# Kernel tuning notes

Measured on AMD Instinct MI355X. Metric: run time of the kernel, lower is better.

## Reference

```python
import jax, jax.numpy as jnp
import numpy as np

H = 256
V = 50257
L = 2048
B = 32


def setup_inputs() -> dict:
    key = jax.random.key(0)
    ks = jax.random.split(key, 14)
    s = 0.05  # weight scale
    return {
        "tokens": jax.random.randint(ks[0], (B,), 0, V),
        "hidden": jax.random.normal(ks[1], (1, B, H), jnp.float32),
        "cell": jax.random.normal(ks[2], (1, B, H), jnp.float32),
        "encoder_outputs": jax.random.normal(ks[3], (B, L, H), jnp.float32),
        "emb_table": jax.random.normal(ks[4], (V, H), jnp.float32) * s,
        "W_attn": jax.random.normal(ks[5], (H, 2 * H), jnp.float32) * s,
        "b_attn": jax.random.normal(ks[6], (H,), jnp.float32) * s,
        "v": jax.random.normal(ks[7], (H,), jnp.float32) * s,
        "W_ih": jax.random.normal(ks[8], (4 * H, 2 * H), jnp.float32) * s,
        "b_ih": jax.random.normal(ks[9], (4 * H,), jnp.float32) * s,
        "W_hh": jax.random.normal(ks[10], (4 * H, H), jnp.float32) * s,
        "b_hh": jax.random.normal(ks[11], (4 * H,), jnp.float32) * s,
        "W_out": jax.random.normal(ks[12], (V, 2 * H), jnp.float32) * s,
        "b_out": jax.random.normal(ks[13], (V,), jnp.float32) * s,
    }


def reference(tokens, hidden, cell, encoder_outputs, emb_table, W_attn, b_attn, v,
              W_ih, b_ih, W_hh, b_hh, W_out, b_out):
    # embedded: (B, H); dropout is identity in eval mode
    embedded = emb_table[tokens]
    h_last = hidden[-1]  # (B, H)

    # Bahdanau-style energy: attn(cat(h, e)) then dot with v (NO tanh, per source)
    # split the 2H-input linear into hidden part and encoder part
    Wh, We = W_attn[:, :H], W_attn[:, H:]
    eh = h_last @ Wh.T                                      # (B, H)
    ee = jnp.einsum('blh,kh->blk', encoder_outputs, We)     # (B, L, H)
    energy = eh[:, None, :] + ee + b_attn                   # (B, L, H)
    scores = energy @ v                                     # (B, L)
    attn_weights = jax.nn.softmax(scores, axis=-1)          # (B, L)

    # context = bmm(attn_weights, encoder_outputs)
    attn_applied = jnp.einsum('bl,blh->bh', attn_weights, encoder_outputs)  # (B, H)

    # single-step LSTM, input = cat(embedded, context): (B, 2H)
    x = jnp.concatenate([embedded, attn_applied], axis=-1)
    gates = x @ W_ih.T + b_ih + hidden[0] @ W_hh.T + b_hh   # (B, 4H)
    i_g, f_g, g_g, o_g = jnp.split(gates, 4, axis=-1)
    c_new = jax.nn.sigmoid(f_g) * cell[0] + jax.nn.sigmoid(i_g) * jnp.tanh(g_g)
    h_new = jax.nn.sigmoid(o_g) * jnp.tanh(c_new)           # (B, H)

    # output projection on cat(lstm_out, context): (B, 2H) -> (B, V)
    logits = jnp.concatenate([h_new, attn_applied], axis=-1) @ W_out.T + b_out
    log_probs = jax.nn.log_softmax(logits, axis=-1)

    return (log_probs, h_new[None], c_new[None], attn_weights[:, None, :])
```

## Files before the change

### kernel.cpp

```cpp
#include <hip/hip_runtime.h>
#include <cstddef>

#define H   256
#define L   2048
#define B   32
#define V   50257
#define H2  512
#define H4  1024
#define CH  64
#define NCH (L/CH)

#define LP_OFF 0
#define HN_OFF (B*V)
#define CN_OFF (HN_OFF + B*H)
#define AW_OFF (CN_OFF + B*H)

#define WS_WP    0
#define WS_XG    (WS_WP + 32*256)
#define WS_XL    (WS_XG + B*H2)
#define WS_S     (WS_XL + B*H2)
#define WS_AV    (WS_S + B*L)
#define WS_AM    (WS_AV + B*NCH*H)
#define WS_AZ    (WS_AM + B*NCH)
#define WS_GATES (WS_AZ + B*NCH)
#define WS_PM    (WS_GATES + B*H4)
#define WS_PZ    (WS_PM + 12800)
#define WS_M     (WS_PZ + 12800)
#define WS_LZ    (WS_M + 32)

#define NBLK_LOG 393

typedef __attribute__((ext_vector_type(8))) short bf16x8;
typedef __attribute__((ext_vector_type(4))) float f32x4;

__device__ inline unsigned short f2bf(float f) {
    unsigned u = __builtin_bit_cast(unsigned, f);
    u += 0x7FFFu + ((u >> 16) & 1u);
    return (unsigned short)(u >> 16);
}

__global__ __launch_bounds__(256) void k_prep(const float* __restrict__ W_attn,
                                              const float* __restrict__ v,
                                              float* __restrict__ ws) {
    int p = blockIdx.x, t = threadIdx.x;
    const float* base = W_attn + H + t;
    float acc = 0.f;
    #pragma unroll
    for (int kk = 0; kk < 8; kk++) {
        int k = p * 8 + kk;
        acc += v[k] * base[(size_t)k * H2];
    }
    ws[WS_WP + p * 256 + t] = acc;
}

__global__ __launch_bounds__(256) void k_attn_flash(const float* __restrict__ enc,
                                                    float* __restrict__ ws) {
    int bid = blockIdx.x;
    int b = bid >> 5, chunk = bid & (NCH - 1);
    int t = threadIdx.x;
    int wave = t >> 6, lane = t & 63;
    int g = lane >> 4, u = lane & 15;
    __shared__ float w_s[256];
    __shared__ float s_lds[CH];
    __shared__ float p_lds[CH];
    __shared__ float red[CH];
    __shared__ float vec_lds[4][256];

    float wsum = 0.f;
    #pragma unroll 8
    for (int p = 0; p < 32; p++) wsum += ws[WS_WP + p * 256 + t];
    w_s[t] = wsum;
    __syncthreads();

    size_t rowbase = (size_t)b * L + chunk * CH;
    const float4* w4s = (const float4*)w_s;
    float4 w0 = w4s[u], w1 = w4s[16 + u], w2 = w4s[32 + u], w3 = w4s[48 + u];

    #pragma unroll
    for (int ir = 0; ir < 4; ir++) {
        int rl = wave * 16 + ir * 4 + g;
        const float4* e4 = (const float4*)(enc + (rowbase + rl) * H);
        float4 a0 = e4[u], a1 = e4[16 + u], a2 = e4[32 + u], a3 = e4[48 + u];
        float p = a0.x * w0.x + a0.y * w0.y + a0.z * w0.z + a0.w * w0.w
                + a1.x * w1.x + a1.y * w1.y + a1.z * w1.z + a1.w * w1.w
                + a2.x * w2.x + a2.y * w2.y + a2.z * w2.z + a2.w * w2.w
                + a3.x * w3.x + a3.y * w3.y + a3.z * w3.z + a3.w * w3.w;
        p += __shfl_down(p, 8); p += __shfl_down(p, 4);
        p += __shfl_down(p, 2); p += __shfl_down(p, 1);
        if (u == 0) s_lds[rl] = p;
    }
    __syncthreads();

    if (t < CH) red[t] = s_lds[t];
    __syncthreads();
    for (int off = 32; off; off >>= 1) { if (t < off) red[t] = fmaxf(red[t], red[t + off]); __syncthreads(); }
    float m = red[0];
    __syncthreads();
    if (t < CH) {
        float e = __expf(s_lds[t] - m);
        p_lds[t] = e; red[t] = e;
        ws[WS_S + rowbase + t] = s_lds[t];
    }
    __syncthreads();
    for (int off = 32; off; off >>= 1) { if (t < off) red[t] += red[t + off]; __syncthreads(); }

    float4 acc = make_float4(0.f, 0.f, 0.f, 0.f);
    const float4* ebase = (const float4*)(enc + (rowbase + wave * 16) * H);
    #pragma unroll 4
    for (int i = 0; i < 16; i++) {
        float p = p_lds[wave * 16 + i];
        float4 a = ebase[i * 64 + lane];
        acc.x += p * a.x; acc.y += p * a.y; acc.z += p * a.z; acc.w += p * a.w;
    }
    *(float4*)&vec_lds[wave][lane * 4] = acc;
    __syncthreads();
    ws[WS_AV + (size_t)bid * 256 + t] = vec_lds[0][t] + vec_lds[1][t] + vec_lds[2][t] + vec_lds[3][t];
    if (t == 0) { ws[WS_AM + bid] = m; ws[WS_AZ + bid] = red[0]; }
}

__global__ __launch_bounds__(256) void k_attn_comb(const int* __restrict__ tokens,
                                                   const float* __restrict__ emb,
                                                   float* __restrict__ ws,
                                                   float* __restrict__ out) {
    int b = blockIdx.x, t = threadIdx.x;
    __shared__ float mc[NCH], zc[NCH];
    if (t < NCH) { mc[t] = ws[WS_AM + b * NCH + t]; zc[t] = ws[WS_AZ + b * NCH + t]; }
    __syncthreads();
    float M = -1e30f;
    #pragma unroll
    for (int c = 0; c < NCH; c++) M = fmaxf(M, mc[c]);
    float Z = 0.f;
    #pragma unroll
    for (int c = 0; c < NCH; c++) Z += zc[c] * __expf(mc[c] - M);
    float inv = 1.f / Z;
    float acc = 0.f;
    #pragma unroll 8
    for (int c = 0; c < NCH; c++) acc += __expf(mc[c] - M) * ws[WS_AV + (size_t)(b * NCH + c) * 256 + t];
    acc *= inv;
    ws[WS_XG + b * H2 + H + t] = acc;
    ws[WS_XL + b * H2 + H + t] = acc;
    int tok = tokens[b];
    ws[WS_XG + b * H2 + t] = emb[(size_t)tok * H + t];
    #pragma unroll
    for (int j = 0; j < 8; j++) {
        int l = t + 256 * j;
        out[AW_OFF + (size_t)b * L + l] = __expf(ws[WS_S + (size_t)b * L + l] - M) * inv;
    }
}

__global__ __launch_bounds__(256) void k_gates(const float* __restrict__ W_ih, const float* __restrict__ b_ih,
                                               const float* __restrict__ W_hh, const float* __restrict__ b_hh,
                                               const float* __restrict__ hidden, float* __restrict__ ws) {
    int t = threadIdx.x;
    int wave = t >> 6, lane = t & 63;
    int o = blockIdx.x * 4 + wave;
    int b = o >> 10, j = o & 1023;
    const float4* wi = (const float4*)(W_ih + (size_t)j * H2);
    const float4* xg = (const float4*)(ws + WS_XG + (size_t)b * H2);
    float4 a0 = wi[lane * 2], a1 = wi[lane * 2 + 1];
    float4 x0 = xg[lane * 2], x1 = xg[lane * 2 + 1];
    float p = a0.x * x0.x + a0.y * x0.y + a0.z * x0.z + a0.w * x0.w
            + a1.x * x1.x + a1.y * x1.y + a1.z * x1.z + a1.w * x1.w;
    const float4* wh = (const float4*)(W_hh + (size_t)j * H);
    const float4* hp = (const float4*)(hidden + (size_t)b * H);
    float4 a2 = wh[lane], x2 = hp[lane];
    p += a2.x * x2.x + a2.y * x2.y + a2.z * x2.z + a2.w * x2.w;
    #pragma unroll
    for (int off = 32; off; off >>= 1) p += __shfl_down(p, off);
    if (lane == 0) ws[WS_GATES + o] = p + b_ih[j] + b_hh[j];
}

__global__ __launch_bounds__(256) void k_lstm(const float* __restrict__ cell,
                                              float* __restrict__ ws, float* __restrict__ out) {
    int b = blockIdx.x, t = threadIdx.x;
    const float* g = ws + WS_GATES + (size_t)b * H4;
    float ig = g[t], fg = g[H + t], gg = g[2 * H + t], og = g[3 * H + t];
    float c = cell[(size_t)b * H + t];
    float si = 1.f / (1.f + expf(-ig));
    float sf = 1.f / (1.f + expf(-fg));
    float so = 1.f / (1.f + expf(-og));
    float cn = sf * c + si * tanhf(gg);
    float hn = so * tanhf(cn);
    out[HN_OFF + b * H + t] = hn;
    out[CN_OFF + b * H + t] = cn;
    ws[WS_XL + b * H2 + t] = hn;
}

__global__ __launch_bounds__(256) void k_logits(const float* __restrict__ W_out,
                                                const float* __restrict__ b_out,
                                                float* __restrict__ ws,
                                                float* __restrict__ out) {
    __shared__ unsigned short Xl[32 * 520];
    int t = threadIdx.x;
    const float4* xl4 = (const float4*)(ws + WS_XL);
    #pragma unroll
    for (int it = 0; it < 16; it++) {
        int fi = t + 256 * it;
        int b = fi >> 7, kq = fi & 127;
        float4 xv = xl4[b * 128 + kq];
        unsigned p0 = (unsigned)f2bf(xv.x) | ((unsigned)f2bf(xv.y) << 16);
        unsigned p1 = (unsigned)f2bf(xv.z) | ((unsigned)f2bf(xv.w) << 16);
        unsigned* dst = (unsigned*)&Xl[b * 520 + kq * 4];
        dst[0] = p0; dst[1] = p1;
    }
    __syncthreads();

    int wave = t >> 6, lane = t & 63, quad = lane >> 4, m = lane & 15;
    int rbase = blockIdx.x * 128 + wave * 32;
    f32x4 zero4 = {0.f, 0.f, 0.f, 0.f};
    f32x4 acc[2][2];
    acc[0][0] = zero4; acc[0][1] = zero4; acc[1][0] = zero4; acc[1][1] = zero4;

    int r0 = rbase + m;
    int r1 = rbase + 16 + m;
    bool v0 = r0 < V, v1 = r1 < V;
    const float* wp0 = W_out + (size_t)r0 * H2 + quad * 8;
    const float* wp1 = W_out + (size_t)r1 * H2 + quad * 8;

    for (int kp = 0; kp < 16; kp++) {
        int k0 = kp * 32;
        bf16x8 a0 = {0,0,0,0,0,0,0,0}, a1 = {0,0,0,0,0,0,0,0};
        if (v0) {
            float4 lo = *(const float4*)(wp0 + k0);
            float4 hi = *(const float4*)(wp0 + k0 + 4);
            a0[0]=(short)f2bf(lo.x); a0[1]=(short)f2bf(lo.y); a0[2]=(short)f2bf(lo.z); a0[3]=(short)f2bf(lo.w);
            a0[4]=(short)f2bf(hi.x); a0[5]=(short)f2bf(hi.y); a0[6]=(short)f2bf(hi.z); a0[7]=(short)f2bf(hi.w);
        }
        if (v1) {
            float4 lo = *(const float4*)(wp1 + k0);
            float4 hi = *(const float4*)(wp1 + k0 + 4);
            a1[0]=(short)f2bf(lo.x); a1[1]=(short)f2bf(lo.y); a1[2]=(short)f2bf(lo.z); a1[3]=(short)f2bf(lo.w);
            a1[4]=(short)f2bf(hi.x); a1[5]=(short)f2bf(hi.y); a1[6]=(short)f2bf(hi.z); a1[7]=(short)f2bf(hi.w);
        }
        bf16x8 b0 = *(bf16x8*)&Xl[(size_t)m * 520 + k0 + quad * 8];
        bf16x8 b1 = *(bf16x8*)&Xl[(size_t)(16 + m) * 520 + k0 + quad * 8];
        acc[0][0] = __builtin_amdgcn_mfma_f32_16x16x32_bf16(a0, b0, acc[0][0], 0, 0, 0);
        acc[0][1] = __builtin_amdgcn_mfma_f32_16x16x32_bf16(a0, b1, acc[0][1], 0, 0, 0);
        acc[1][0] = __builtin_amdgcn_mfma_f32_16x16x32_bf16(a1, b0, acc[1][0], 0, 0, 0);
        acc[1][1] = __builtin_amdgcn_mfma_f32_16x16x32_bf16(a1, b1, acc[1][1], 0, 0, 0);
    }

    float val[2][2][4];
    #pragma unroll
    for (int s = 0; s < 2; s++) {
        #pragma unroll
        for (int i = 0; i < 4; i++) {
            int rr = rbase + s * 16 + quad * 4 + i;
            float bo = (rr < V) ? b_out[rr] : 0.f;
            #pragma unroll
            for (int nt = 0; nt < 2; nt++) {
                float vv = acc[s][nt][i] + bo;
                if (rr < V) {
                    int bcol = nt * 16 + m;
                    out[(size_t)bcol * V + rr] = vv;
                    val[s][nt][i] = vv;
                } else {
                    val[s][nt][i] = -1e30f;
                }
            }
        }
    }
    float pm[2], pz[2];
    #pragma unroll
    for (int nt = 0; nt < 2; nt++) {
        float mx = -1e30f;
        #pragma unroll
        for (int s = 0; s < 2; s++)
            #pragma unroll
            for (int i = 0; i < 4; i++) mx = fmaxf(mx, val[s][nt][i]);
        float sm = 0.f;
        #pragma unroll
        for (int s = 0; s < 2; s++)
            #pragma unroll
            for (int i = 0; i < 4; i++) sm += __expf(val[s][nt][i] - mx);
        pm[nt] = mx; pz[nt] = sm;
    }
    #pragma unroll
    for (int off = 16; off <= 32; off <<= 1) {
        #pragma unroll
        for (int nt = 0; nt < 2; nt++) {
            float om = __shfl_xor(pm[nt], off);
            float oz = __shfl_xor(pz[nt], off);
            float nm = fmaxf(pm[nt], om);
            pz[nt] = pz[nt] * __expf(pm[nt] - nm) + oz * __expf(om - nm);
            pm[nt] = nm;
        }
    }
    __syncthreads();
    float* red = (float*)Xl;
    if (quad == 0) {
        #pragma unroll
        for (int nt = 0; nt < 2; nt++) {
            red[wave * 32 + nt * 16 + m]       = pm[nt];
            red[128 + wave * 32 + nt * 16 + m] = pz[nt];
        }
    }
    __syncthreads();
    if (t < 32) {
        float mf = -1e30f;
        #pragma unroll
        for (int w = 0; w < 4; w++) mf = fmaxf(mf, red[w * 32 + t]);
        float z = 0.f;
        #pragma unroll
        for (int w = 0; w < 4; w++) z += red[128 + w * 32 + t] * __expf(red[w * 32 + t] - mf);
        ws[WS_PM + t * 400 + blockIdx.x] = mf;
        ws[WS_PZ + t * 400 + blockIdx.x] = z;
    }
}

__global__ __launch_bounds__(256) void k_lsm_comb(float* __restrict__ ws) {
    int b = blockIdx.x, t = threadIdx.x;
    float m = -1e30f, z = 0.f;
    for (int i = t; i < NBLK_LOG; i += 256) {
        float mi = ws[WS_PM + b * 400 + i];
        float zi = ws[WS_PZ + b * 400 + i];
        float nm = fmaxf(m, mi);
        z = z * __expf(m - nm) + zi * __expf(mi - nm);
        m = nm;
    }
    __shared__ float rm[256], rz[256];
    rm[t] = m; rz[t] = z; __syncthreads();
    for (int off = 128; off; off >>= 1) {
        if (t < off) {
            float m2 = rm[t + off], z2 = rz[t + off];
            float nm = fmaxf(rm[t], m2);
            rz[t] = rz[t] * __expf(rm[t] - nm) + z2 * __expf(m2 - nm);
            rm[t] = nm;
        }
        __syncthreads();
    }
    if (t == 0) { ws[WS_M + b] = rm[0]; ws[WS_LZ + b] = logf(rz[0]); }
}

__global__ __launch_bounds__(256) void k_lsm_final(const float* __restrict__ ws, float* __restrict__ out) {
    int b = blockIdx.y;
    int r = blockIdx.x * 256 + threadIdx.x;
    if (r < V) {
        size_t i = (size_t)b * V + r;
        out[i] = out[i] - ws[WS_M + b] - ws[WS_LZ + b];
    }
}

extern "C" void kernel_launch(void* const* d_in, const int* in_sizes, int n_in,
                              void* d_out, int out_size, void* d_ws, size_t ws_size,
                              hipStream_t stream) {
    const int*   tokens = (const int*)d_in[0];
    const float* hidden = (const float*)d_in[1];
    const float* cell   = (const float*)d_in[2];
    const float* enc    = (const float*)d_in[3];
    const float* emb    = (const float*)d_in[4];
    const float* W_attn = (const float*)d_in[5];
    const float* v      = (const float*)d_in[7];
    const float* W_ih   = (const float*)d_in[8];
    const float* b_ih   = (const float*)d_in[9];
    const float* W_hh   = (const float*)d_in[10];
    const float* b_hh   = (const float*)d_in[11];
    const float* W_out  = (const float*)d_in[12];
    const float* b_out  = (const float*)d_in[13];
    float* out = (float*)d_out;
    float* ws  = (float*)d_ws;

    k_prep<<<32, 256, 0, stream>>>(W_attn, v, ws);
    k_attn_flash<<<B * NCH, 256, 0, stream>>>(enc, ws);
    k_attn_comb<<<B, 256, 0, stream>>>(tokens, emb, ws, out);
    k_gates<<<(B * H4) / 4, 256, 0, stream>>>(W_ih, b_ih, W_hh, b_hh, hidden, ws);
    k_lstm<<<B, 256, 0, stream>>>(cell, ws, out);
    k_logits<<<NBLK_LOG, 256, 0, stream>>>(W_out, b_out, ws, out);
    k_lsm_comb<<<B, 256, 0, stream>>>(ws);
    k_lsm_final<<<dim3((V + 255) / 256, B), 256, 0, stream>>>(ws, out);
}
```

Before: 289.8 us.

## Fuse attention prep, LSTM gates and log-softmax stages to cut kernel launches

Folds the W_attn·v precompute into each attention block, which now recomputes it redundantly. The attention combine, gate GEMV and LSTM cell are merged into one kernel of 512 blocks, each handling 16 hidden units per batch row. The log-softmax combine is merged into the final normalization, so each block re-reduces the 393 partials and then handles 1024 columns. In k_logits the out-of-range rows are clamped instead of branched on, which drops divergent loads. Together these go from eight launches to four, at the cost of redundant recomputation (256x256 W_attn reads per attention block, partial reductions repeated per block).

```diff
diff --git a/kernel.cpp b/kernel.cpp
--- a/kernel.cpp
+++ b/kernel.cpp
@@ -15,18 +15,13 @@
 #define CN_OFF (HN_OFF + B*H)
 #define AW_OFF (CN_OFF + B*H)
 
-#define WS_WP    0
-#define WS_XG    (WS_WP + 32*256)
-#define WS_XL    (WS_XG + B*H2)
+#define WS_XL    0
 #define WS_S     (WS_XL + B*H2)
 #define WS_AV    (WS_S + B*L)
 #define WS_AM    (WS_AV + B*NCH*H)
 #define WS_AZ    (WS_AM + B*NCH)
-#define WS_GATES (WS_AZ + B*NCH)
-#define WS_PM    (WS_GATES + B*H4)
+#define WS_PM    (WS_AZ + B*NCH)
 #define WS_PZ    (WS_PM + 12800)
-#define WS_M     (WS_PZ + 12800)
-#define WS_LZ    (WS_M + 32)
 
 #define NBLK_LOG 393
 
@@ -39,37 +34,34 @@
     return (unsigned short)(u >> 16);
 }
 
-__global__ __launch_bounds__(256) void k_prep(const float* __restrict__ W_attn,
+__global__ __launch_bounds__(256) void k_attn(const float* __restrict__ W_attn,
                                               const float* __restrict__ v,
+                                              const float* __restrict__ enc,
                                               float* __restrict__ ws) {
-    int p = blockIdx.x, t = threadIdx.x;
-    const float* base = W_attn + H + t;
-    float acc = 0.f;
-    #pragma unroll
-    for (int kk = 0; kk < 8; kk++) {
-        int k = p * 8 + kk;
-        acc += v[k] * base[(size_t)k * H2];
-    }
-    ws[WS_WP + p * 256 + t] = acc;
-}
-
-__global__ __launch_bounds__(256) void k_attn_flash(const float* __restrict__ enc,
-                                                    float* __restrict__ ws) {
     int bid = blockIdx.x;
     int b = bid >> 5, chunk = bid & (NCH - 1);
     int t = threadIdx.x;
     int wave = t >> 6, lane = t & 63;
     int g = lane >> 4, u = lane & 15;
-    __shared__ float w_s[256];
+    __shared__ float v_s[H];
+    __shared__ float w_s[H];
     __shared__ float s_lds[CH];
     __shared__ float p_lds[CH];
     __shared__ float red[CH];
     __shared__ float vec_lds[4][256];
 
-    float wsum = 0.f;
-    #pragma unroll 8
-    for (int p = 0; p < 32; p++) wsum += ws[WS_WP + p * 256 + t];
-    w_s[t] = wsum;
+    v_s[t] = v[t];
+    __syncthreads();
+    {
+        const float* base = W_attn + H + t;
+        float wa = 0.f, wb = 0.f;
+        #pragma unroll 8
+        for (int k = 0; k < H; k += 2) {
+            wa += v_s[k]     * base[(size_t)k * H2];
+            wb += v_s[k + 1] * base[(size_t)(k + 1) * H2];
+        }
+        w_s[t] = wa + wb;
+    }
     __syncthreads();
 
     size_t rowbase = (size_t)b * L + chunk * CH;
@@ -118,14 +110,31 @@
     if (t == 0) { ws[WS_AM + bid] = m; ws[WS_AZ + bid] = red[0]; }
 }
 
-__global__ __launch_bounds__(256) void k_attn_comb(const int* __restrict__ tokens,
-                                                   const float* __restrict__ emb,
-                                                   float* __restrict__ ws,
-                                                   float* __restrict__ out) {
-    int b = blockIdx.x, t = threadIdx.x;
+__global__ __launch_bounds__(256) void k_fuse(const int* __restrict__ tokens,
+                                              const float* __restrict__ emb,
+                                              const float* __restrict__ hidden,
+                                              const float* __restrict__ cell,
+                                              const float* __restrict__ W_ih,
+                                              const float* __restrict__ b_ih,
+                                              const float* __restrict__ W_hh,
+                                              const float* __restrict__ b_hh,
+                                              float* __restrict__ ws,
+                                              float* __restrict__ out) {
+    int blk = blockIdx.x;
+    int b = blk >> 4, s = blk & 15;
+    int t = threadIdx.x;
+    int wave = t >> 6, lane = t & 63;
     __shared__ float mc[NCH], zc[NCH];
+    __shared__ float xs[H2];
+    __shared__ float hs[H];
+    __shared__ float gl[64];
+
     if (t < NCH) { mc[t] = ws[WS_AM + b * NCH + t]; zc[t] = ws[WS_AZ + b * NCH + t]; }
-    __syncthreads();
+    hs[t] = hidden[(size_t)b * H + t];
+    int tok = tokens[b];
+    xs[t] = emb[(size_t)tok * H + t];
+    __syncthreads();
+
     float M = -1e30f;
     #pragma unroll
     for (int c = 0; c < NCH; c++) M = fmaxf(M, mc[c]);
@@ -135,55 +144,52 @@
     float inv = 1.f / Z;
     float acc = 0.f;
     #pragma unroll 8
-    for (int c = 0; c < NCH; c++) acc += __expf(mc[c] - M) * ws[WS_AV + (size_t)(b * NCH + c) * 256 + t];
+    for (int c = 0; c < NCH; c++) acc += __expf(mc[c] - M) * ws[WS_AV + (size_t)(b * NCH + c) * H + t];
     acc *= inv;
-    ws[WS_XG + b * H2 + H + t] = acc;
-    ws[WS_XL + b * H2 + H + t] = acc;
-    int tok = tokens[b];
-    ws[WS_XG + b * H2 + t] = emb[(size_t)tok * H + t];
-    #pragma unroll
-    for (int j = 0; j < 8; j++) {
-        int l = t + 256 * j;
-        out[AW_OFF + (size_t)b * L + l] = __expf(ws[WS_S + (size_t)b * L + l] - M) * inv;
-    }
-}
-
-__global__ __launch_bounds__(256) void k_gates(const float* __restrict__ W_ih, const float* __restrict__ b_ih,
-                                               const float* __restrict__ W_hh, const float* __restrict__ b_hh,
-                                               const float* __restrict__ hidden, float* __restrict__ ws) {
-    int t = threadIdx.x;
-    int wave = t >> 6, lane = t & 63;
-    int o = blockIdx.x * 4 + wave;
-    int b = o >> 10, j = o & 1023;
-    const float4* wi = (const float4*)(W_ih + (size_t)j * H2);
-    const float4* xg = (const float4*)(ws + WS_XG + (size_t)b * H2);
-    float4 a0 = wi[lane * 2], a1 = wi[lane * 2 + 1];
-    float4 x0 = xg[lane * 2], x1 = xg[lane * 2 + 1];
-    float p = a0.x * x0.x + a0.y * x0.y + a0.z * x0.z + a0.w * x0.w
-            + a1.x * x1.x + a1.y * x1.y + a1.z * x1.z + a1.w * x1.w;
-    const float4* wh = (const float4*)(W_hh + (size_t)j * H);
-    const float4* hp = (const float4*)(hidden + (size_t)b * H);
-    float4 a2 = wh[lane], x2 = hp[lane];
-    p += a2.x * x2.x + a2.y * x2.y + a2.z * x2.z + a2.w * x2.w;
-    #pragma unroll
-    for (int off = 32; off; off >>= 1) p += __shfl_down(p, off);
-    if (lane == 0) ws[WS_GATES + o] = p + b_ih[j] + b_hh[j];
-}
-
-__global__ __launch_bounds__(256) void k_lstm(const float* __restrict__ cell,
-                                              float* __restrict__ ws, float* __restrict__ out) {
-    int b = blockIdx.x, t = threadIdx.x;
-    const float* g = ws + WS_GATES + (size_t)b * H4;
-    float ig = g[t], fg = g[H + t], gg = g[2 * H + t], og = g[3 * H + t];
-    float c = cell[(size_t)b * H + t];
-    float si = 1.f / (1.f + expf(-ig));
-    float sf = 1.f / (1.f + expf(-fg));
-    float so = 1.f / (1.f + expf(-og));
-    float cn = sf * c + si * tanhf(gg);
-    float hn = so * tanhf(cn);
-    out[HN_OFF + b * H + t] = hn;
-    out[CN_OFF + b * H + t] = cn;
-    ws[WS_XL + b * H2 + t] = hn;
+    xs[H + t] = acc;
+    if (s == 0) {
+        ws[WS_XL + b * H2 + H + t] = acc;
+        #pragma unroll
+        for (int j = 0; j < 8; j++) {
+            int l = t + 256 * j;
+            out[AW_OFF + (size_t)b * L + l] = __expf(ws[WS_S + (size_t)b * L + l] - M) * inv;
+        }
+    }
+    __syncthreads();
+
+    int ts = s * 16;
+    const float4* xs4 = (const float4*)xs;
+    const float4* hs4 = (const float4*)hs;
+    float4 x0 = xs4[lane * 2], x1 = xs4[lane * 2 + 1];
+    float4 xh = hs4[lane];
+    for (int it = 0; it < 16; it++) {
+        int j = (wave << 8) + ts + it;
+        const float4* wi = (const float4*)(W_ih + (size_t)j * H2);
+        float4 a0 = wi[lane * 2], a1 = wi[lane * 2 + 1];
+        const float4* wh = (const float4*)(W_hh + (size_t)j * H);
+        float4 a2 = wh[lane];
+        float p = a0.x * x0.x + a0.y * x0.y + a0.z * x0.z + a0.w * x0.w
+                + a1.x * x1.x + a1.y * x1.y + a1.z * x1.z + a1.w * x1.w
+                + a2.x * xh.x + a2.y * xh.y + a2.z * xh.z + a2.w * xh.w;
+        #pragma unroll
+        for (int off = 32; off; off >>= 1) p += __shfl_down(p, off);
+        if (lane == 0) gl[wave * 16 + it] = p + b_ih[j] + b_hh[j];
+    }
+    __syncthreads();
+
+    if (t < 16) {
+        int tt = ts + t;
+        float ig = gl[t], fg = gl[16 + t], gg = gl[32 + t], og = gl[48 + t];
+        float c = cell[(size_t)b * H + tt];
+        float si = 1.f / (1.f + expf(-ig));
+        float sf = 1.f / (1.f + expf(-fg));
+        float so = 1.f / (1.f + expf(-og));
+        float cn = sf * c + si * tanhf(gg);
+        float hn = so * tanhf(cn);
+        out[HN_OFF + b * H + tt] = hn;
+        out[CN_OFF + b * H + tt] = cn;
+        ws[WS_XL + b * H2 + tt] = hn;
+    }
 }
 
 __global__ __launch_bounds__(256) void k_logits(const float* __restrict__ W_out,
@@ -213,25 +219,22 @@
 
     int r0 = rbase + m;
     int r1 = rbase + 16 + m;
-    bool v0 = r0 < V, v1 = r1 < V;
-    const float* wp0 = W_out + (size_t)r0 * H2 + quad * 8;
-    const float* wp1 = W_out + (size_t)r1 * H2 + quad * 8;
+    int r0c = r0 < V ? r0 : V - 1;
+    int r1c = r1 < V ? r1 : V - 1;
+    const float* wp0 = W_out + (size_t)r0c * H2 + quad * 8;
+    const float* wp1 = W_out + (size_t)r1c * H2 + quad * 8;
 
     for (int kp = 0; kp < 16; kp++) {
         int k0 = kp * 32;
-        bf16x8 a0 = {0,0,0,0,0,0,0,0}, a1 = {0,0,0,0,0,0,0,0};
-        if (v0) {
-            float4 lo = *(const float4*)(wp0 + k0);
-            float4 hi = *(const float4*)(wp0 + k0 + 4);
-            a0[0]=(short)f2bf(lo.x); a0[1]=(short)f2bf(lo.y); a0[2]=(short)f2bf(lo.z); a0[3]=(short)f2bf(lo.w);
-            a0[4]=(short)f2bf(hi.x); a0[5]=(short)f2bf(hi.y); a0[6]=(short)f2bf(hi.z); a0[7]=(short)f2bf(hi.w);
-        }
-        if (v1) {
-            float4 lo = *(const float4*)(wp1 + k0);
-            float4 hi = *(const float4*)(wp1 + k0 + 4);
-            a1[0]=(short)f2bf(lo.x); a1[1]=(short)f2bf(lo.y); a1[2]=(short)f2bf(lo.z); a1[3]=(short)f2bf(lo.w);
-            a1[4]=(short)f2bf(hi.x); a1[5]=(short)f2bf(hi.y); a1[6]=(short)f2bf(hi.z); a1[7]=(short)f2bf(hi.w);
-        }
+        float4 lo0 = *(const float4*)(wp0 + k0);
+        float4 hi0 = *(const float4*)(wp0 + k0 + 4);
+        float4 lo1 = *(const float4*)(wp1 + k0);
+        float4 hi1 = *(const float4*)(wp1 + k0 + 4);
+        bf16x8 a0, a1;
+        a0[0]=(short)f2bf(lo0.x); a0[1]=(short)f2bf(lo0.y); a0[2]=(short)f2bf(lo0.z); a0[3]=(short)f2bf(lo0.w);
+        a0[4]=(short)f2bf(hi0.x); a0[5]=(short)f2bf(hi0.y); a0[6]=(short)f2bf(hi0.z); a0[7]=(short)f2bf(hi0.w);
+        a1[0]=(short)f2bf(lo1.x); a1[1]=(short)f2bf(lo1.y); a1[2]=(short)f2bf(lo1.z); a1[3]=(short)f2bf(lo1.w);
+        a1[4]=(short)f2bf(hi1.x); a1[5]=(short)f2bf(hi1.y); a1[6]=(short)f2bf(hi1.z); a1[7]=(short)f2bf(hi1.w);
         bf16x8 b0 = *(bf16x8*)&Xl[(size_t)m * 520 + k0 + quad * 8];
         bf16x8 b1 = *(bf16x8*)&Xl[(size_t)(16 + m) * 520 + k0 + quad * 8];
         acc[0][0] = __builtin_amdgcn_mfma_f32_16x16x32_bf16(a0, b0, acc[0][0], 0, 0, 0);
@@ -308,8 +311,10 @@
     }
 }
 
-__global__ __launch_bounds__(256) void k_lsm_comb(float* __restrict__ ws) {
-    int b = blockIdx.x, t = threadIdx.x;
+__global__ __launch_bounds__(256) void k_lsm_final(const float* __restrict__ ws,
+                                                   float* __restrict__ out) {
+    int b = blockIdx.y, t = threadIdx.x;
+    __shared__ float rm[256], rz[256];
     float m = -1e30f, z = 0.f;
     for (int i = t; i < NBLK_LOG; i += 256) {
         float mi = ws[WS_PM + b * 400 + i];
@@ -318,7 +323,6 @@
         z = z * __expf(m - nm) + zi * __expf(mi - nm);
         m = nm;
     }
-    __shared__ float rm[256], rz[256];
     rm[t] = m; rz[t] = z; __syncthreads();
     for (int off = 128; off; off >>= 1) {
         if (t < off) {
@@ -329,15 +333,15 @@
         }
         __syncthreads();
     }
-    if (t == 0) { ws[WS_M + b] = rm[0]; ws[WS_LZ + b] = logf(rz[0]); }
-}
-
-__global__ __launch_bounds__(256) void k_lsm_final(const float* __restrict__ ws, float* __restrict__ out) {
-    int b = blockIdx.y;
-    int r = blockIdx.x * 256 + threadIdx.x;
-    if (r < V) {
-        size_t i = (size_t)b * V + r;
-        out[i] = out[i] - ws[WS_M + b] - ws[WS_LZ + b];
+    float M = rm[0], LZ = logf(rz[0]);
+    int rbase = blockIdx.x * 1024 + t;
+    #pragma unroll
+    for (int j = 0; j < 4; j++) {
+        int r = rbase + 256 * j;
+        if (r < V) {
+            size_t i = (size_t)b * V + r;
+            out[i] = out[i] - M - LZ;
+        }
     }
 }
 
@@ -360,12 +364,8 @@
     float* out = (float*)d_out;
     float* ws  = (float*)d_ws;
 
-    k_prep<<<32, 256, 0, stream>>>(W_attn, v, ws);
-    k_attn_flash<<<B * NCH, 256, 0, stream>>>(enc, ws);
-    k_attn_comb<<<B, 256, 0, stream>>>(tokens, emb, ws, out);
-    k_gates<<<(B * H4) / 4, 256, 0, stream>>>(W_ih, b_ih, W_hh, b_hh, hidden, ws);
-    k_lstm<<<B, 256, 0, stream>>>(cell, ws, out);
+    k_attn<<<B * NCH, 256, 0, stream>>>(W_attn, v, enc, ws);
+    k_fuse<<<B * 16, 256, 0, stream>>>(tokens, emb, hidden, cell, W_ih, b_ih, W_hh, b_hh, ws, out);
     k_logits<<<NBLK_LOG, 256, 0, stream>>>(W_out, b_out, ws, out);
-    k_lsm_comb<<<B, 256, 0, stream>>>(ws);
-    k_lsm_final<<<dim3((V + 255) / 256, B), 256, 0, stream>>>(ws, out);
-}
+    k_lsm_final<<<dim3((V + 1023) / 1024, B), 256, 0, stream>>>(ws, out);
+}
```

After: 297.2 us. 2.6% more time.

## Halve logits rows per block and software-prefetch W_out three steps ahead

Applied to the files above, without the earlier changes.

The logits GEMV kernel now gives each wave 16 vocabulary rows instead of 32, doubling the grid to 786 blocks, and the partial-softmax workspace grows to match. The K loop is fully unrolled with a 3-deep register prefetch of W_out rows, and out-of-range rows are clamped rather than branched, so more global loads are in flight while the MFMAs run. This targets latency hiding in the memory-bound W_out stream. In exchange it adds more blocks, re-stages X into LDS for every block, and doubles the per-block partial results that the combine kernel has to reduce.

```diff
diff --git a/kernel.cpp b/kernel.cpp
--- a/kernel.cpp
+++ b/kernel.cpp
@@ -24,11 +24,11 @@
 #define WS_AZ    (WS_AM + B*NCH)
 #define WS_GATES (WS_AZ + B*NCH)
 #define WS_PM    (WS_GATES + B*H4)
-#define WS_PZ    (WS_PM + 12800)
-#define WS_M     (WS_PZ + 12800)
+#define WS_PZ    (WS_PM + 32*800)
+#define WS_M     (WS_PZ + 32*800)
 #define WS_LZ    (WS_M + 32)
 
-#define NBLK_LOG 393
+#define NBLK_LOG 786
 
 typedef __attribute__((ext_vector_type(8))) short bf16x8;
 typedef __attribute__((ext_vector_type(4))) float f32x4;
@@ -191,88 +191,68 @@
                                                 float* __restrict__ ws,
                                                 float* __restrict__ out) {
     __shared__ unsigned short Xl[32 * 520];
+    __shared__ float red2[256];
     int t = threadIdx.x;
     const float4* xl4 = (const float4*)(ws + WS_XL);
     #pragma unroll
     for (int it = 0; it < 16; it++) {
         int fi = t + 256 * it;
-        int b = fi >> 7, kq = fi & 127;
-        float4 xv = xl4[b * 128 + kq];
+        int bb = fi >> 7, kq = fi & 127;
+        float4 xv = xl4[bb * 128 + kq];
         unsigned p0 = (unsigned)f2bf(xv.x) | ((unsigned)f2bf(xv.y) << 16);
         unsigned p1 = (unsigned)f2bf(xv.z) | ((unsigned)f2bf(xv.w) << 16);
-        unsigned* dst = (unsigned*)&Xl[b * 520 + kq * 4];
+        unsigned* dst = (unsigned*)&Xl[bb * 520 + kq * 4];
         dst[0] = p0; dst[1] = p1;
     }
     __syncthreads();
 
     int wave = t >> 6, lane = t & 63, quad = lane >> 4, m = lane & 15;
-    int rbase = blockIdx.x * 128 + wave * 32;
-    f32x4 zero4 = {0.f, 0.f, 0.f, 0.f};
-    f32x4 acc[2][2];
-    acc[0][0] = zero4; acc[0][1] = zero4; acc[1][0] = zero4; acc[1][1] = zero4;
-
+    int rbase = blockIdx.x * 64 + wave * 16;
     int r0 = rbase + m;
-    int r1 = rbase + 16 + m;
-    bool v0 = r0 < V, v1 = r1 < V;
-    const float* wp0 = W_out + (size_t)r0 * H2 + quad * 8;
-    const float* wp1 = W_out + (size_t)r1 * H2 + quad * 8;
-
+    int rc = r0 < V ? r0 : V - 1;
+    const float4* wq = (const float4*)(W_out + (size_t)rc * H2 + quad * 8);
+
+    f32x4 acc0 = {0.f, 0.f, 0.f, 0.f}, acc1 = {0.f, 0.f, 0.f, 0.f};
+
+    float4 pl0 = wq[0],  ph0 = wq[1];
+    float4 pl1 = wq[8],  ph1 = wq[9];
+    float4 pl2 = wq[16], ph2 = wq[17];
+    #pragma unroll
     for (int kp = 0; kp < 16; kp++) {
         int k0 = kp * 32;
-        bf16x8 a0 = {0,0,0,0,0,0,0,0}, a1 = {0,0,0,0,0,0,0,0};
-        if (v0) {
-            float4 lo = *(const float4*)(wp0 + k0);
-            float4 hi = *(const float4*)(wp0 + k0 + 4);
-            a0[0]=(short)f2bf(lo.x); a0[1]=(short)f2bf(lo.y); a0[2]=(short)f2bf(lo.z); a0[3]=(short)f2bf(lo.w);
-            a0[4]=(short)f2bf(hi.x); a0[5]=(short)f2bf(hi.y); a0[6]=(short)f2bf(hi.z); a0[7]=(short)f2bf(hi.w);
-        }
-        if (v1) {
-            float4 lo = *(const float4*)(wp1 + k0);
-            float4 hi = *(const float4*)(wp1 + k0 + 4);
-            a1[0]=(short)f2bf(lo.x); a1[1]=(short)f2bf(lo.y); a1[2]=(short)f2bf(lo.z); a1[3]=(short)f2bf(lo.w);
-            a1[4]=(short)f2bf(hi.x); a1[5]=(short)f2bf(hi.y); a1[6]=(short)f2bf(hi.z); a1[7]=(short)f2bf(hi.w);
-        }
+        bf16x8 a;
+        a[0]=(short)f2bf(pl0.x); a[1]=(short)f2bf(pl0.y); a[2]=(short)f2bf(pl0.z); a[3]=(short)f2bf(pl0.w);
+        a[4]=(short)f2bf(ph0.x); a[5]=(short)f2bf(ph0.y); a[6]=(short)f2bf(ph0.z); a[7]=(short)f2bf(ph0.w);
         bf16x8 b0 = *(bf16x8*)&Xl[(size_t)m * 520 + k0 + quad * 8];
         bf16x8 b1 = *(bf16x8*)&Xl[(size_t)(16 + m) * 520 + k0 + quad * 8];
-        acc[0][0] = __builtin_amdgcn_mfma_f32_16x16x32_bf16(a0, b0, acc[0][0], 0, 0, 0);
-        acc[0][1] = __builtin_amdgcn_mfma_f32_16x16x32_bf16(a0, b1, acc[0][1], 0, 0, 0);
-        acc[1][0] = __builtin_amdgcn_mfma_f32_16x16x32_bf16(a1, b0, acc[1][0], 0, 0, 0);
-        acc[1][1] = __builtin_amdgcn_mfma_f32_16x16x32_bf16(a1, b1, acc[1][1], 0, 0, 0);
-    }
-
-    float val[2][2][4];
-    #pragma unroll
-    for (int s = 0; s < 2; s++) {
-        #pragma unroll
-        for (int i = 0; i < 4; i++) {
-            int rr = rbase + s * 16 + quad * 4 + i;
-            float bo = (rr < V) ? b_out[rr] : 0.f;
-            #pragma unroll
-            for (int nt = 0; nt < 2; nt++) {
-                float vv = acc[s][nt][i] + bo;
-                if (rr < V) {
-                    int bcol = nt * 16 + m;
-                    out[(size_t)bcol * V + rr] = vv;
-                    val[s][nt][i] = vv;
-                } else {
-                    val[s][nt][i] = -1e30f;
-                }
-            }
-        }
+        acc0 = __builtin_amdgcn_mfma_f32_16x16x32_bf16(a, b0, acc0, 0, 0, 0);
+        acc1 = __builtin_amdgcn_mfma_f32_16x16x32_bf16(a, b1, acc1, 0, 0, 0);
+        pl0 = pl1; ph0 = ph1;
+        pl1 = pl2; ph1 = ph2;
+        if (kp < 13) { pl2 = wq[(kp + 3) * 8]; ph2 = wq[(kp + 3) * 8 + 1]; }
+    }
+
+    float val[2][4];
+    #pragma unroll
+    for (int i = 0; i < 4; i++) {
+        int rr = rbase + quad * 4 + i;
+        float bo = (rr < V) ? b_out[rr] : 0.f;
+        float v0 = acc0[i] + bo, v1 = acc1[i] + bo;
+        if (rr < V) {
+            out[(size_t)m * V + rr]        = v0;
+            out[(size_t)(16 + m) * V + rr] = v1;
+            val[0][i] = v0; val[1][i] = v1;
+        } else { val[0][i] = -1e30f; val[1][i] = -1e30f; }
     }
     float pm[2], pz[2];
     #pragma unroll
     for (int nt = 0; nt < 2; nt++) {
         float mx = -1e30f;
         #pragma unroll
-        for (int s = 0; s < 2; s++)
-            #pragma unroll
-            for (int i = 0; i < 4; i++) mx = fmaxf(mx, val[s][nt][i]);
+        for (int i = 0; i < 4; i++) mx = fmaxf(mx, val[nt][i]);
         float sm = 0.f;
         #pragma unroll
-        for (int s = 0; s < 2; s++)
-            #pragma unroll
-            for (int i = 0; i < 4; i++) sm += __expf(val[s][nt][i] - mx);
+        for (int i = 0; i < 4; i++) sm += __expf(val[nt][i] - mx);
         pm[nt] = mx; pz[nt] = sm;
     }
     #pragma unroll
@@ -287,24 +267,23 @@
         }
     }
     __syncthreads();
-    float* red = (float*)Xl;
     if (quad == 0) {
         #pragma unroll
         for (int nt = 0; nt < 2; nt++) {
-            red[wave * 32 + nt * 16 + m]       = pm[nt];
-            red[128 + wave * 32 + nt * 16 + m] = pz[nt];
+            red2[wave * 32 + nt * 16 + m]       = pm[nt];
+            red2[128 + wave * 32 + nt * 16 + m] = pz[nt];
         }
     }
     __syncthreads();
     if (t < 32) {
         float mf = -1e30f;
         #pragma unroll
-        for (int w = 0; w < 4; w++) mf = fmaxf(mf, red[w * 32 + t]);
+        for (int w = 0; w < 4; w++) mf = fmaxf(mf, red2[w * 32 + t]);
         float z = 0.f;
         #pragma unroll
-        for (int w = 0; w < 4; w++) z += red[128 + w * 32 + t] * __expf(red[w * 32 + t] - mf);
-        ws[WS_PM + t * 400 + blockIdx.x] = mf;
-        ws[WS_PZ + t * 400 + blockIdx.x] = z;
+        for (int w = 0; w < 4; w++) z += red2[128 + w * 32 + t] * __expf(red2[w * 32 + t] - mf);
+        ws[WS_PM + t * 800 + blockIdx.x] = mf;
+        ws[WS_PZ + t * 800 + blockIdx.x] = z;
     }
 }
 
@@ -312,8 +291,8 @@
     int b = blockIdx.x, t = threadIdx.x;
     float m = -1e30f, z = 0.f;
     for (int i = t; i < NBLK_LOG; i += 256) {
-        float mi = ws[WS_PM + b * 400 + i];
-        float zi = ws[WS_PZ + b * 400 + i];
+        float mi = ws[WS_PM + b * 800 + i];
+        float zi = ws[WS_PZ + b * 800 + i];
         float nm = fmaxf(m, mi);
         z = z * __expf(m - nm) + zi * __expf(mi - nm);
         m = nm;
```

After: 294.7 us. No clear change (+1.7%).

## Pre-convert W_out to bf16 in the attention kernel and read bf16 in logits

Applied to the files above, without the earlier changes.

The attention kernel now also converts all of W_out from fp32 to bf16 into a new workspace region, split evenly across its 1024 blocks. The logits kernel then reads half as many bytes of bf16 weights and skips per-element conversion, and clamps out-of-range rows instead of branching. The intent is to move the conversion off the logits critical path and let it run alongside the latency-bound attention pass. The cost is that every call still reads the full fp32 matrix and adds a 51 MB write plus a second read. An fp32-reading fallback kernel runs when the workspace is too small.

```diff
diff --git a/kernel.cpp b/kernel.cpp
--- a/kernel.cpp
+++ b/kernel.cpp
@@ -27,8 +27,11 @@
 #define WS_PZ    (WS_PM + 12800)
 #define WS_M     (WS_PZ + 12800)
 #define WS_LZ    (WS_M + 32)
+#define WS_WB    (WS_LZ + 32)
+#define WS_TOTAL (WS_WB + (V*H2)/2)
 
 #define NBLK_LOG 393
+#define TOTF4    ((V * H2) / 4)
 
 typedef __attribute__((ext_vector_type(8))) short bf16x8;
 typedef __attribute__((ext_vector_type(4))) float f32x4;
@@ -54,7 +57,9 @@
 }
 
 __global__ __launch_bounds__(256) void k_attn_flash(const float* __restrict__ enc,
-                                                    float* __restrict__ ws) {
+                                                    const float* __restrict__ W_out,
+                                                    float* __restrict__ ws,
+                                                    int do_warm) {
     int bid = blockIdx.x;
     int b = bid >> 5, chunk = bid & (NCH - 1);
     int t = threadIdx.x;
@@ -116,6 +121,22 @@
     __syncthreads();
     ws[WS_AV + (size_t)bid * 256 + t] = vec_lds[0][t] + vec_lds[1][t] + vec_lds[2][t] + vec_lds[3][t];
     if (t == 0) { ws[WS_AM + bid] = m; ws[WS_AZ + bid] = red[0]; }
+
+    if (do_warm) {
+        int per = (TOTF4 + 1023) / 1024;
+        int start = bid * per;
+        int end = start + per;
+        if (end > TOTF4) end = TOTF4;
+        const float4* w4 = (const float4*)W_out;
+        ushort4* wb = (ushort4*)(ws + WS_WB);
+        #pragma unroll 4
+        for (int i = start + t; i < end; i += 256) {
+            float4 x = w4[i];
+            ushort4 o;
+            o.x = f2bf(x.x); o.y = f2bf(x.y); o.z = f2bf(x.z); o.w = f2bf(x.w);
+            wb[i] = o;
+        }
+    }
 }
 
 __global__ __launch_bounds__(256) void k_attn_comb(const int* __restrict__ tokens,
@@ -186,8 +207,7 @@
     ws[WS_XL + b * H2 + t] = hn;
 }
 
-__global__ __launch_bounds__(256) void k_logits(const float* __restrict__ W_out,
-                                                const float* __restrict__ b_out,
+__global__ __launch_bounds__(256) void k_logits(const float* __restrict__ b_out,
                                                 float* __restrict__ ws,
                                                 float* __restrict__ out) {
     __shared__ unsigned short Xl[32 * 520];
@@ -196,11 +216,11 @@
     #pragma unroll
     for (int it = 0; it < 16; it++) {
         int fi = t + 256 * it;
-        int b = fi >> 7, kq = fi & 127;
-        float4 xv = xl4[b * 128 + kq];
+        int bb = fi >> 7, kq = fi & 127;
+        float4 xv = xl4[bb * 128 + kq];
         unsigned p0 = (unsigned)f2bf(xv.x) | ((unsigned)f2bf(xv.y) << 16);
         unsigned p1 = (unsigned)f2bf(xv.z) | ((unsigned)f2bf(xv.w) << 16);
-        unsigned* dst = (unsigned*)&Xl[b * 520 + kq * 4];
+        unsigned* dst = (unsigned*)&Xl[bb * 520 + kq * 4];
         dst[0] = p0; dst[1] = p1;
     }
     __syncthreads();
@@ -213,25 +233,135 @@
 
     int r0 = rbase + m;
     int r1 = rbase + 16 + m;
-    bool v0 = r0 < V, v1 = r1 < V;
-    const float* wp0 = W_out + (size_t)r0 * H2 + quad * 8;
-    const float* wp1 = W_out + (size_t)r1 * H2 + quad * 8;
+    int r0c = r0 < V ? r0 : V - 1;
+    int r1c = r1 < V ? r1 : V - 1;
+    const unsigned short* wb = (const unsigned short*)(ws + WS_WB);
+    const unsigned short* wp0 = wb + (size_t)r0c * H2 + quad * 8;
+    const unsigned short* wp1 = wb + (size_t)r1c * H2 + quad * 8;
 
     for (int kp = 0; kp < 16; kp++) {
         int k0 = kp * 32;
-        bf16x8 a0 = {0,0,0,0,0,0,0,0}, a1 = {0,0,0,0,0,0,0,0};
-        if (v0) {
-            float4 lo = *(const float4*)(wp0 + k0);
-            float4 hi = *(const float4*)(wp0 + k0 + 4);
-            a0[0]=(short)f2bf(lo.x); a0[1]=(short)f2bf(lo.y); a0[2]=(short)f2bf(lo.z); a0[3]=(short)f2bf(lo.w);
-            a0[4]=(short)f2bf(hi.x); a0[5]=(short)f2bf(hi.y); a0[6]=(short)f2bf(hi.z); a0[7]=(short)f2bf(hi.w);
-        }
-        if (v1) {
-            float4 lo = *(const float4*)(wp1 + k0);
-            float4 hi = *(const float4*)(wp1 + k0 + 4);
-            a1[0]=(short)f2bf(lo.x); a1[1]=(short)f2bf(lo.y); a1[2]=(short)f2bf(lo.z); a1[3]=(short)f2bf(lo.w);
-            a1[4]=(short)f2bf(hi.x); a1[5]=(short)f2bf(hi.y); a1[6]=(short)f2bf(hi.z); a1[7]=(short)f2bf(hi.w);
-        }
+        bf16x8 a0 = *(const bf16x8*)(wp0 + k0);
+        bf16x8 a1 = *(const bf16x8*)(wp1 + k0);
+        bf16x8 b0 = *(bf16x8*)&Xl[(size_t)m * 520 + k0 + quad * 8];
+        bf16x8 b1 = *(bf16x8*)&Xl[(size_t)(16 + m) * 520 + k0 + quad * 8];
+        acc[0][0] = __builtin_amdgcn_mfma_f32_16x16x32_bf16(a0, b0, acc[0][0], 0, 0, 0);
+        acc[0][1] = __builtin_amdgcn_mfma_f32_16x16x32_bf16(a0, b1, acc[0][1], 0, 0, 0);
+        acc[1][0] = __builtin_amdgcn_mfma_f32_16x16x32_bf16(a1, b0, acc[1][0], 0, 0, 0);
+        acc[1][1] = __builtin_amdgcn_mfma_f32_16x16x32_bf16(a1, b1, acc[1][1], 0, 0, 0);
+    }
+
+    float val[2][2][4];
+    #pragma unroll
+    for (int s = 0; s < 2; s++) {
+        #pragma unroll
+        for (int i = 0; i < 4; i++) {
+            int rr = rbase + s * 16 + quad * 4 + i;
+            float bo = (rr < V) ? b_out[rr] : 0.f;
+            #pragma unroll
+            for (int nt = 0; nt < 2; nt++) {
+                float vv = acc[s][nt][i] + bo;
+                if (rr < V) {
+                    int bcol = nt * 16 + m;
+                    out[(size_t)bcol * V + rr] = vv;
+                    val[s][nt][i] = vv;
+                } else {
+                    val[s][nt][i] = -1e30f;
+                }
+            }
+        }
+    }
+    float pm[2], pz[2];
+    #pragma unroll
+    for (int nt = 0; nt < 2; nt++) {
+        float mx = -1e30f;
+        #pragma unroll
+        for (int s = 0; s < 2; s++)
+            #pragma unroll
+            for (int i = 0; i < 4; i++) mx = fmaxf(mx, val[s][nt][i]);
+        float sm = 0.f;
+        #pragma unroll
+        for (int s = 0; s < 2; s++)
+            #pragma unroll
+            for (int i = 0; i < 4; i++) sm += __expf(val[s][nt][i] - mx);
+        pm[nt] = mx; pz[nt] = sm;
+    }
+    #pragma unroll
+    for (int off = 16; off <= 32; off <<= 1) {
+        #pragma unroll
+        for (int nt = 0; nt < 2; nt++) {
+            float om = __shfl_xor(pm[nt], off);
+            float oz = __shfl_xor(pz[nt], off);
+            float nm = fmaxf(pm[nt], om);
+            pz[nt] = pz[nt] * __expf(pm[nt] - nm) + oz * __expf(om - nm);
+            pm[nt] = nm;
+        }
+    }
+    __syncthreads();
+    float* red = (float*)Xl;
+    if (quad == 0) {
+        #pragma unroll
+        for (int nt = 0; nt < 2; nt++) {
+            red[wave * 32 + nt * 16 + m]       = pm[nt];
+            red[128 + wave * 32 + nt * 16 + m] = pz[nt];
+        }
+    }
+    __syncthreads();
+    if (t < 32) {
+        float mf = -1e30f;
+        #pragma unroll
+        for (int w = 0; w < 4; w++) mf = fmaxf(mf, red[w * 32 + t]);
+        float z = 0.f;
+        #pragma unroll
+        for (int w = 0; w < 4; w++) z += red[128 + w * 32 + t] * __expf(red[w * 32 + t] - mf);
+        ws[WS_PM + t * 400 + blockIdx.x] = mf;
+        ws[WS_PZ + t * 400 + blockIdx.x] = z;
+    }
+}
+
+__global__ __launch_bounds__(256) void k_logits_fb(const float* __restrict__ W_out,
+                                                   const float* __restrict__ b_out,
+                                                   float* __restrict__ ws,
+                                                   float* __restrict__ out) {
+    __shared__ unsigned short Xl[32 * 520];
+    int t = threadIdx.x;
+    const float4* xl4 = (const float4*)(ws + WS_XL);
+    #pragma unroll
+    for (int it = 0; it < 16; it++) {
+        int fi = t + 256 * it;
+        int bb = fi >> 7, kq = fi & 127;
+        float4 xv = xl4[bb * 128 + kq];
+        unsigned p0 = (unsigned)f2bf(xv.x) | ((unsigned)f2bf(xv.y) << 16);
+        unsigned p1 = (unsigned)f2bf(xv.z) | ((unsigned)f2bf(xv.w) << 16);
+        unsigned* dst = (unsigned*)&Xl[bb * 520 + kq * 4];
+        dst[0] = p0; dst[1] = p1;
+    }
+    __syncthreads();
+
+    int wave = t >> 6, lane = t & 63, quad = lane >> 4, m = lane & 15;
+    int rbase = blockIdx.x * 128 + wave * 32;
+    f32x4 zero4 = {0.f, 0.f, 0.f, 0.f};
+    f32x4 acc[2][2];
+    acc[0][0] = zero4; acc[0][1] = zero4; acc[1][0] = zero4; acc[1][1] = zero4;
+
+    int r0 = rbase + m;
+    int r1 = rbase + 16 + m;
+    int r0c = r0 < V ? r0 : V - 1;
+    int r1c = r1 < V ? r1 : V - 1;
+    const float* wp0 = W_out + (size_t)r0c * H2 + quad * 8;
+    const float* wp1 = W_out + (size_t)r1c * H2 + quad * 8;
+
+    for (int kp = 0; kp < 16; kp++) {
+        int k0 = kp * 32;
+        float4 lo0 = *(const float4*)(wp0 + k0);
+        float4 hi0 = *(const float4*)(wp0 + k0 + 4);
+        float4 lo1 = *(const float4*)(wp1 + k0);
+        float4 hi1 = *(const float4*)(wp1 + k0 + 4);
+        bf16x8 a0, a1;
+        a0[0]=(short)f2bf(lo0.x); a0[1]=(short)f2bf(lo0.y); a0[2]=(short)f2bf(lo0.z); a0[3]=(short)f2bf(lo0.w);
+        a0[4]=(short)f2bf(hi0.x); a0[5]=(short)f2bf(hi0.y); a0[6]=(short)f2bf(hi0.z); a0[7]=(short)f2bf(hi0.w);
+        a1[0]=(short)f2bf(lo1.x); a1[1]=(short)f2bf(lo1.y); a1[2]=(short)f2bf(lo1.z); a1[3]=(short)f2bf(lo1.w);
+        a1[4]=(short)f2bf(hi1.x); a1[5]=(short)f2bf(hi1.y); a1[6]=(short)f2bf(hi1.z); a1[7]=(short)f2bf(hi1.w);
         bf16x8 b0 = *(bf16x8*)&Xl[(size_t)m * 520 + k0 + quad * 8];
         bf16x8 b1 = *(bf16x8*)&Xl[(size_t)(16 + m) * 520 + k0 + quad * 8];
         acc[0][0] = __builtin_amdgcn_mfma_f32_16x16x32_bf16(a0, b0, acc[0][0], 0, 0, 0);
@@ -360,12 +490,18 @@
     float* out = (float*)d_out;
     float* ws  = (float*)d_ws;
 
+    int warm = (ws_size >= (size_t)WS_TOTAL * sizeof(float)) ? 1 : 0;
+
     k_prep<<<32, 256, 0, stream>>>(W_attn, v, ws);
-    k_attn_flash<<<B * NCH, 256, 0, stream>>>(enc, ws);
+    k_attn_flash<<<B * NCH, 256, 0, stream>>>(enc, W_out, ws, warm);
     k_attn_comb<<<B, 256, 0, stream>>>(tokens, emb, ws, out);
     k_gates<<<(B * H4) / 4, 256, 0, stream>>>(W_ih, b_ih, W_hh, b_hh, hidden, ws);
     k_lstm<<<B, 256, 0, stream>>>(cell, ws, out);
-    k_logits<<<NBLK_LOG, 256, 0, stream>>>(W_out, b_out, ws, out);
+    if (warm) {
+        k_logits<<<NBLK_LOG, 256, 0, stream>>>(b_out, ws, out);
+    } else {
+        k_logits_fb<<<NBLK_LOG, 256, 0, stream>>>(W_out, b_out, ws, out);
+    }
     k_lsm_comb<<<B, 256, 0, stream>>>(ws);
     k_lsm_final<<<dim3((V + 255) / 256, B), 256, 0, stream>>>(ws, out);
 }
```

After: 304.9 us. 5.2% more time.
